# Optimization experiments

Hardware: AMD Instinct MI355X
Metric: run time of the kernel (lower is better)

## Reference

```python
import jax, jax.numpy as jnp
import numpy as np
from jax import lax

# pywt db4 filters (8 taps)
_DEC_LO = np.array([-0.010597401784997278, 0.032883011666982945, 0.030841381835986965,
                    -0.18703481171888114, -0.02798376941698385, 0.6308807679295904,
                    0.7148465705525415, 0.23037781330885523])
_DEC_HI = np.array([-0.23037781330885523, 0.7148465705525415, -0.6308807679295904,
                    -0.02798376941698385, 0.18703481171888114, 0.030841381835986965,
                    -0.032883011666982945, -0.010597401784997278])
_REC_LO = _DEC_LO[::-1].copy()
_REC_HI = _DEC_HI[::-1].copy()
_L = 8  # filter length
LEVELS = 4


def _dwt_level(x):
    # x: (M, n) -> (cA, cD) each (M, (n+_L-1)//2), pywt 'symmetric' mode
    xe = jnp.pad(x, ((0, 0), (_L - 1, _L - 1)), mode='symmetric')[:, 1:]
    ker = jnp.stack([_DEC_LO[::-1], _DEC_HI[::-1]]).astype(x.dtype)[:, None, :]  # (2,1,L)
    y = lax.conv_general_dilated(xe[:, None, :], ker, (2,), 'VALID')  # (M,2,m)
    return y[:, 0], y[:, 1]


def _idwt_level(ca, cd, out_len):
    # inverse DWT, cropped to out_len (matches length of next-finer approximation)
    inp = jnp.stack([ca, cd], axis=1)  # (M,2,m)
    ker = jnp.stack([_REC_LO[::-1], _REC_HI[::-1]]).astype(ca.dtype)[None]  # (1,2,L)
    y = lax.conv_general_dilated(inp, ker, (1,), [(_L - 1, _L - 1)], lhs_dilation=(2,))
    return y[:, 0, _L - 2:_L - 2 + out_len]


def setup_inputs() -> dict:
    key = jax.random.key(0)
    k1, k2, k3, k4 = jax.random.split(key, 4)
    B, N, C = 32, 8192, 64
    m = N
    for _ in range(LEVELS):
        m = (m + _L - 1) // 2  # 518
    scale = 1.0 / (C * C)
    return {
        'x': jax.random.normal(k1, (B, N, C), jnp.float32),
        'w1': scale * jax.random.uniform(k2, (C, C, m), jnp.float32),
        'w2': scale * jax.random.uniform(k3, (C, C, m), jnp.float32),
        'dense_kernel': jax.random.normal(k4, (C, C), jnp.float32) / jnp.sqrt(C).astype(jnp.float32),
        'dense_bias': jnp.zeros((C,), jnp.float32),
    }


def reference(x, w1, w2, dense_kernel, dense_bias):
    B, N, C = x.shape
    xc = jnp.transpose(x, (0, 2, 1)).reshape(B * C, N)  # per-(batch,channel) signals
    # analysis: multi-level DWT
    lens, details = [], []
    a = xc
    for _ in range(LEVELS):
        lens.append(a.shape[1])
        a, d = _dwt_level(a)
        details.append(d)
    m = a.shape[1]
    # channel mixing on coarsest approximation and coarsest detail (WNO kernel)
    a = jnp.einsum('bim,iom->bom', a.reshape(B, C, m), w1).reshape(B * C, m)
    details[-1] = jnp.einsum('bim,iom->bom', details[-1].reshape(B, C, m), w2).reshape(B * C, m)
    # synthesis: multi-level IDWT
    for j in range(LEVELS - 1, -1, -1):
        a = _idwt_level(a, details[j], lens[j])
    y = jnp.transpose(a.reshape(B, C, N), (0, 2, 1))
    shortcut = x @ dense_kernel + dense_bias  # Dense 1x1 shortcut
    out = y + shortcut
    return out * jnp.tanh(jax.nn.softplus(out))  # mish
```

## Files before the change

kernel.cpp:

```cpp
#include <hip/hip_runtime.h>
#include <hip/hip_bf16.h>
#include <stdint.h>

typedef __attribute__((ext_vector_type(8))) short short8;
typedef __attribute__((ext_vector_type(4))) float floatx4;

__device__ __constant__ float c_DL[8] = {
    -0.010597401784997278f, 0.032883011666982945f, 0.030841381835986965f,
    -0.18703481171888114f, -0.02798376941698385f, 0.6308807679295904f,
    0.7148465705525415f, 0.23037781330885523f};
__device__ __constant__ float c_DH[8] = {
    -0.23037781330885523f, 0.7148465705525415f, -0.6308807679295904f,
    -0.02798376941698385f, 0.18703481171888114f, 0.030841381835986965f,
    -0.032883011666982945f, -0.010597401784997278f};
__device__ __constant__ float c_RL[8] = {
    0.23037781330885523f, 0.7148465705525415f, 0.6308807679295904f,
    -0.02798376941698385f, -0.18703481171888114f, 0.030841381835986965f,
    0.032883011666982945f, -0.010597401784997278f};
__device__ __constant__ float c_RH[8] = {
    -0.010597401784997278f, -0.032883011666982945f, 0.030841381835986965f,
    0.18703481171888114f, -0.02798376941698385f, -0.6308807679295904f,
    0.7148465705525415f, -0.23037781330885523f};

__device__ __forceinline__ float bflo(uint32_t u) { return __uint_as_float(u << 16); }
__device__ __forceinline__ float bfhi(uint32_t u) { return __uint_as_float(u & 0xffff0000u); }
__device__ __forceinline__ float ldf(const float* p, size_t i) { return p[i]; }
__device__ __forceinline__ float ldf(const __hip_bfloat16* p, size_t i) { return __bfloat162float(p[i]); }
__device__ __forceinline__ void stf(float* p, size_t i, float v) { p[i] = v; }
__device__ __forceinline__ void stf(__hip_bfloat16* p, size_t i, float v) { p[i] = __float2bfloat16(v); }
__device__ __forceinline__ short f2bs(float f) {
  __hip_bfloat16 h = __float2bfloat16(f);
  return *reinterpret_cast<short*>(&h);
}

__device__ __forceinline__ int reflect_idx(int t, int n) {
  if (t < 0) t = -1 - t;
  if (t >= n) t = 2 * n - 1 - t;
  return t;
}

#define S1R 4100
#define S2R 2056

#define NT1 134
__global__ __launch_bounds__(256) void k_dwt_first(const float* __restrict__ x,
                                                   __hip_bfloat16* __restrict__ outa,
                                                   __hip_bfloat16* __restrict__ outd) {
  const int b = blockIdx.y;
  const int k0 = blockIdx.x * 64;
  const int tid = threadIdx.x;
  __shared__ float xs[NT1 * 65];

  const float4* x4 = (const float4*)x;
  for (int idx = tid; idx < NT1 * 16; idx += 256) {
    int nl = idx >> 4, cq = idx & 15;
    int t = 2 * k0 - 6 + nl;
    int n = reflect_idx(t, 8192);
    float4 v = x4[((size_t)b * 8192 + n) * 16 + cq];
    float* d = &xs[nl * 65 + 4 * cq];
    d[0] = v.x; d[1] = v.y; d[2] = v.z; d[3] = v.w;
  }
  __syncthreads();

  const int kk = tid & 63;
  const int k = k0 + kk;
  if (k >= 4099) return;
  for (int c = (tid >> 6); c < 64; c += 4) {
    float lo = 0.f, hi = 0.f;
#pragma unroll
    for (int j = 0; j < 8; ++j) {
      float v = xs[(2 * kk + 7 - j) * 65 + c];
      lo += c_DL[j] * v;
      hi += c_DH[j] * v;
    }
    size_t s = (size_t)b * 64 + c;
    outa[s * S1R + k] = __float2bfloat16(lo);
    outd[s * S1R + k] = __float2bfloat16(hi);
  }
}

__global__ __launch_bounds__(256) void k_ana234(const __hip_bfloat16* __restrict__ a1,
                                                __hip_bfloat16* __restrict__ d2o,
                                                float* __restrict__ d3o,
                                                float* __restrict__ a4o,
                                                float* __restrict__ d4o) {
  const int r = blockIdx.x;
  const int tid = threadIdx.x;
  __shared__ float s1[4100];
  __shared__ float s2[2054];
  __shared__ float s3[1032];

  const uint2* row2 = (const uint2*)(a1 + (size_t)r * S1R);
  for (int i = tid; i < 1025; i += 256) {
    uint2 u = row2[i];
    int e = 4 * i;
    s1[e] = bflo(u.x); s1[e + 1] = bfhi(u.x);
    s1[e + 2] = bflo(u.y); s1[e + 3] = bfhi(u.y);
  }
  __syncthreads();

  for (int k = tid; k < 2053; k += 256) {
    float lo = 0.f, hi = 0.f;
    if (k >= 3 && k <= 2048) {
      const float2* p = (const float2*)&s1[2 * k - 6];
      float2 v0 = p[0], v1 = p[1], v2 = p[2], v3 = p[3];
      lo = c_RL[0]*v0.x + c_RL[1]*v0.y + c_RL[2]*v1.x + c_RL[3]*v1.y +
           c_RL[4]*v2.x + c_RL[5]*v2.y + c_RL[6]*v3.x + c_RL[7]*v3.y;
      hi = c_RH[0]*v0.x + c_RH[1]*v0.y + c_RH[2]*v1.x + c_RH[3]*v1.y +
           c_RH[4]*v2.x + c_RH[5]*v2.y + c_RH[6]*v3.x + c_RH[7]*v3.y;
    } else {
#pragma unroll
      for (int j = 0; j < 8; ++j) {
        float v = s1[reflect_idx(2 * k + 1 - j, 4099)];
        lo += c_DL[j] * v; hi += c_DH[j] * v;
      }
    }
    d2o[(size_t)r * S2R + k] = __float2bfloat16(hi);
    s2[k] = lo;
  }
  __syncthreads();

  for (int k = tid; k < 1030; k += 256) {
    float lo = 0.f, hi = 0.f;
    if (k >= 3 && k <= 1025) {
      const float2* p = (const float2*)&s2[2 * k - 6];
      float2 v0 = p[0], v1 = p[1], v2 = p[2], v3 = p[3];
      lo = c_RL[0]*v0.x + c_RL[1]*v0.y + c_RL[2]*v1.x + c_RL[3]*v1.y +
           c_RL[4]*v2.x + c_RL[5]*v2.y + c_RL[6]*v3.x + c_RL[7]*v3.y;
      hi = c_RH[0]*v0.x + c_RH[1]*v0.y + c_RH[2]*v1.x + c_RH[3]*v1.y +
           c_RH[4]*v2.x + c_RH[5]*v2.y + c_RH[6]*v3.x + c_RH[7]*v3.y;
    } else {
#pragma unroll
      for (int j = 0; j < 8; ++j) {
        float v = s2[reflect_idx(2 * k + 1 - j, 2053)];
        lo += c_DL[j] * v; hi += c_DH[j] * v;
      }
    }
    d3o[(size_t)r * 1030 + k] = hi;
    s3[k] = lo;
  }
  __syncthreads();

  for (int k = tid; k < 518; k += 256) {
    float lo = 0.f, hi = 0.f;
    if (k >= 3 && k <= 514) {
      const float2* p = (const float2*)&s3[2 * k - 6];
      float2 v0 = p[0], v1 = p[1], v2 = p[2], v3 = p[3];
      lo = c_RL[0]*v0.x + c_RL[1]*v0.y + c_RL[2]*v1.x + c_RL[3]*v1.y +
           c_RL[4]*v2.x + c_RL[5]*v2.y + c_RL[6]*v3.x + c_RL[7]*v3.y;
      hi = c_RH[0]*v0.x + c_RH[1]*v0.y + c_RH[2]*v1.x + c_RH[3]*v1.y +
           c_RH[4]*v2.x + c_RH[5]*v2.y + c_RH[6]*v3.x + c_RH[7]*v3.y;
    } else {
#pragma unroll
      for (int j = 0; j < 8; ++j) {
        float v = s3[reflect_idx(2 * k + 1 - j, 1030)];
        lo += c_DL[j] * v; hi += c_DH[j] * v;
      }
    }
    a4o[(size_t)r * 518 + k] = lo;
    d4o[(size_t)r * 518 + k] = hi;
  }
}

__global__ __launch_bounds__(256) void k_mix_p(const float* __restrict__ a4,
                                               const float* __restrict__ d4,
                                               const float* __restrict__ w1,
                                               const float* __restrict__ w2,
                                               float* __restrict__ am,
                                               float* __restrict__ dm) {
  const int bx = blockIdx.x;
  const int xcd = bx & 7;
  const int j = bx >> 3;
  const int p = (xcd < 6) ? (xcd * 65 + j) : (390 + (xcd - 6) * 64 + j);

  __shared__ float w1s[4096];
  __shared__ float w2s[4096];
  __shared__ float as[2048];
  __shared__ float ds[2048];

  const int tid = threadIdx.x;
  for (int idx = tid; idx < 4096; idx += 256) {
    w1s[idx] = w1[(size_t)idx * 518 + p];
    w2s[idx] = w2[(size_t)idx * 518 + p];
  }
  for (int idx = tid; idx < 2048; idx += 256) {
    int i = idx >> 5, b = idx & 31;
    as[idx] = a4[(size_t)(b * 64 + i) * 518 + p];
    ds[idx] = d4[(size_t)(b * 64 + i) * 518 + p];
  }
  __syncthreads();

  const int o0 = (tid & 15) * 4;
  const int bq = tid >> 4;
  floatx4 acc0 = {0.f, 0.f, 0.f, 0.f}, acc1 = {0.f, 0.f, 0.f, 0.f};
  floatx4 accd0 = {0.f, 0.f, 0.f, 0.f}, accd1 = {0.f, 0.f, 0.f, 0.f};

#pragma unroll 4
  for (int i = 0; i < 64; ++i) {
    floatx4 wv1 = *(const floatx4*)&w1s[i * 64 + o0];
    floatx4 wv2 = *(const floatx4*)&w2s[i * 64 + o0];
    float a0 = as[i * 32 + bq];
    float a1 = as[i * 32 + bq + 16];
    float dv0 = ds[i * 32 + bq];
    float dv1 = ds[i * 32 + bq + 16];
#pragma unroll
    for (int q = 0; q < 4; ++q) {
      acc0[q] += a0 * wv1[q];
      acc1[q] += a1 * wv1[q];
      accd0[q] += dv0 * wv2[q];
      accd1[q] += dv1 * wv2[q];
    }
  }

#pragma unroll
  for (int q = 0; q < 4; ++q) {
    size_t s0 = (size_t)(bq * 64 + o0 + q) * 518 + p;
    size_t s1 = (size_t)((bq + 16) * 64 + o0 + q) * 518 + p;
    am[s0] = acc0[q];
    am[s1] = acc1[q];
    dm[s0] = accd0[q];
    dm[s1] = accd1[q];
  }
}

__global__ __launch_bounds__(256) void k_syn32(const float* __restrict__ a4m,
                                               const float* __restrict__ d4m,
                                               const float* __restrict__ d3,
                                               __hip_bfloat16* __restrict__ r2out) {
  const int r = blockIdx.x;
  const int tid = threadIdx.x;
  __shared__ float sa[518], sd[518], s3d[1030], r3[1030];
  for (int i = tid; i < 518; i += 256) {
    sa[i] = a4m[(size_t)r * 518 + i];
    sd[i] = d4m[(size_t)r * 518 + i];
  }
  for (int i = tid; i < 1030; i += 256) s3d[i] = d3[(size_t)r * 1030 + i];
  __syncthreads();
  for (int s = tid; s < 1030; s += 256) {
    int u = s >> 1, par = s & 1;
    float acc = 0.f;
#pragma unroll
    for (int t = 0; t < 4; ++t) {
      int i = u + 3 - t;
      float fl = par ? c_RL[2 * t + 1] : c_RL[2 * t];
      float fh = par ? c_RH[2 * t + 1] : c_RH[2 * t];
      acc += fl * sa[i] + fh * sd[i];
    }
    r3[s] = acc;
  }
  __syncthreads();
  for (int s = tid; s < 2053; s += 256) {
    int u = s >> 1, par = s & 1;
    float acc = 0.f;
#pragma unroll
    for (int t = 0; t < 4; ++t) {
      int i = u + 3 - t;
      float fl = par ? c_RL[2 * t + 1] : c_RL[2 * t];
      float fh = par ? c_RH[2 * t + 1] : c_RH[2 * t];
      acc += fl * r3[i] + fh * s3d[i];
    }
    r2out[(size_t)r * S2R + s] = __float2bfloat16(acc);
  }
}

template <typename TCa, typename TCd, typename TOut>
__global__ void k_idwt(const TCa* __restrict__ ca, const TCd* __restrict__ cd,
                       TOut* __restrict__ out, int m, int out_len, int sin, int sout) {
  int s = blockIdx.x * blockDim.x + threadIdx.x;
  if (s >= out_len) return;
  const TCa* pa = ca + (size_t)blockIdx.y * sin;
  const TCd* pd = cd + (size_t)blockIdx.y * sin;
  int u = s >> 1, par = s & 1;
  float acc = 0.f;
#pragma unroll
  for (int t = 0; t < 4; ++t) {
    int i = u + 3 - t;
    float fl = par ? c_RL[2 * t + 1] : c_RL[2 * t];
    float fh = par ? c_RH[2 * t + 1] : c_RH[2 * t];
    acc += fl * ldf(pa, i) + fh * ldf(pd, i);
  }
  stf(out, (size_t)blockIdx.y * sout + s, acc);
}

__global__ __launch_bounds__(256) void k_epilogue(const __hip_bfloat16* __restrict__ r1,
                                                  const __hip_bfloat16* __restrict__ dd1,
                                                  const float* __restrict__ x,
                                                  const float* __restrict__ dk,
                                                  const float* __restrict__ bias,
                                                  float* __restrict__ out) {
  const int b = blockIdx.y;
  const int n0 = blockIdx.x * 64;
  const int u0 = n0 >> 1;
  const int tid = threadIdx.x;
  const int lane = tid & 63;
  const int w = tid >> 6;

  __shared__ __hip_bfloat16 Kt[64 * 72];
  __shared__ float ra[35 * 65];
  __shared__ float rd[35 * 65];

  {
    const float4* dk4 = (const float4*)dk;
    for (int idx = tid; idx < 1024; idx += 256) {
      int c = idx >> 4, o0 = (idx & 15) * 4;
      float4 v = dk4[idx];
      Kt[(o0 + 0) * 72 + c] = __float2bfloat16(v.x);
      Kt[(o0 + 1) * 72 + c] = __float2bfloat16(v.y);
      Kt[(o0 + 2) * 72 + c] = __float2bfloat16(v.z);
      Kt[(o0 + 3) * 72 + c] = __float2bfloat16(v.w);
    }
  }
  {
    int o2 = tid >> 2;
    const __hip_bfloat16* pr = r1 + (size_t)(b * 64 + o2) * S1R + u0;
    const __hip_bfloat16* pd = dd1 + (size_t)(b * 64 + o2) * S1R + u0;
    for (int il = (tid & 3); il < 35; il += 4) {
      ra[il * 65 + o2] = __bfloat162float(pr[il]);
      rd[il * 65 + o2] = __bfloat162float(pd[il]);
    }
  }
  __syncthreads();

  const int m16 = lane & 15;
  const int kq = (lane >> 4) * 8;
  const int nrow = w * 16 + m16;
  const float* xrow = x + ((size_t)b * 8192 + n0 + nrow) * 64;

  floatx4 acc[4];
#pragma unroll
  for (int ot = 0; ot < 4; ++ot) acc[ot] = (floatx4){0.f, 0.f, 0.f, 0.f};

#pragma unroll
  for (int ks = 0; ks < 2; ++ks) {
    float4 xa = *(const float4*)(xrow + ks * 32 + kq);
    float4 xb = *(const float4*)(xrow + ks * 32 + kq + 4);
    short8 af;
    af[0] = f2bs(xa.x); af[1] = f2bs(xa.y); af[2] = f2bs(xa.z); af[3] = f2bs(xa.w);
    af[4] = f2bs(xb.x); af[5] = f2bs(xb.y); af[6] = f2bs(xb.z); af[7] = f2bs(xb.w);
#pragma unroll
    for (int ot = 0; ot < 4; ++ot) {
      short8 bf = *(const short8*)&Kt[(ot * 16 + m16) * 72 + ks * 32 + kq];
      acc[ot] = __builtin_amdgcn_mfma_f32_16x16x32_bf16(af, bf, acc[ot], 0, 0, 0);
    }
  }

  const int rbase = (lane >> 4) * 4;
#pragma unroll
  for (int ot = 0; ot < 4; ++ot) {
    int o_loc = ot * 16 + m16;
    float bo = bias[o_loc];
#pragma unroll
    for (int rg = 0; rg < 4; ++rg) {
      int n_loc = w * 16 + rbase + rg;
      int ul = n_loc >> 1, par = n_loc & 1;
      float wv = 0.f;
#pragma unroll
      for (int t = 0; t < 4; ++t) {
        int i = ul + 3 - t;
        float fl = par ? c_RL[2 * t + 1] : c_RL[2 * t];
        float fh = par ? c_RH[2 * t + 1] : c_RH[2 * t];
        wv += fl * ra[i * 65 + o_loc] + fh * rd[i * 65 + o_loc];
      }
      float v = acc[ot][rg] + wv + bo;
      float e = __expf(fminf(v, 15.f));
      float num = e * (e + 2.f);
      float mm = (v > 15.f) ? v : v * (num / (num + 2.f));
      out[((size_t)b * 8192 + n0 + n_loc) * 64 + o_loc] = mm;
    }
  }
}

extern "C" void kernel_launch(void* const* d_in, const int* in_sizes, int n_in,
                              void* d_out, int out_size, void* d_ws, size_t ws_size,
                              hipStream_t stream) {
  const float* x    = (const float*)d_in[0];
  const float* w1   = (const float*)d_in[1];
  const float* w2   = (const float*)d_in[2];
  const float* dk   = (const float*)d_in[3];
  const float* bias = (const float*)d_in[4];
  float* out = (float*)d_out;

  const size_t R = 2048;

  float* wf = (float*)d_ws;
  float* d3f = wf; wf += R * 1030;
  float* a4f = wf; wf += R * 518;
  float* d4f = wf; wf += R * 518;
  float* a4m = wf; wf += R * 518;
  float* d4m = wf; wf += R * 518;
  __hip_bfloat16* wb = (__hip_bfloat16*)wf;
  __hip_bfloat16* a1b = wb; wb += R * S1R;
  __hip_bfloat16* d1b = wb; wb += R * S1R;
  __hip_bfloat16* a2b = wb; wb += R * S2R;
  __hip_bfloat16* d2b = wb; wb += R * S2R;

  k_dwt_first<<<dim3(65, 32), 256, 0, stream>>>(x, a1b, d1b);
  k_ana234<<<dim3(2048), 256, 0, stream>>>(a1b, d2b, d3f, a4f, d4f);
  k_mix_p<<<dim3(518), 256, 0, stream>>>(a4f, d4f, w1, w2, a4m, d4m);
  k_syn32<<<dim3(2048), 256, 0, stream>>>(a4m, d4m, d3f, a2b);
  k_idwt<__hip_bfloat16, __hip_bfloat16, __hip_bfloat16>
      <<<dim3((4099 + 255) / 256, 2048), 256, 0, stream>>>(a2b, d2b, a1b, 2053, 4099, S2R, S1R);
  k_epilogue<<<dim3(128, 32), 256, 0, stream>>>(a1b, d1b, x, dk, bias, out);
}
```

Baseline: 303.6 us.

## Transpose mixing weights and coarse coefficients to mode-major layout for coalesced loads

Adds a kernel that transposes w1/w2 into mode-major (p, i*64+o) layout on every call. The analysis kernel now writes a4/d4 in mode-major order, with a block-index swizzle so writes are grouped. The mixing kernel then loads contiguous float4 rows per mode and is split in two, one half for approximation and one for detail. This replaces stride-518 gathers in the mixing kernel with coalesced reads, at the cost of an extra pass of about 17 MB over the weights each call and strided writes in the analysis kernel.

```diff
diff --git a/kernel.cpp b/kernel.cpp
--- a/kernel.cpp
+++ b/kernel.cpp
@@ -42,6 +42,28 @@
 #define S1R 4100
 #define S2R 2056
 
+__global__ __launch_bounds__(256) void k_wT(const float* __restrict__ w1,
+                                            const float* __restrict__ w2,
+                                            float* __restrict__ wt1,
+                                            float* __restrict__ wt2) {
+  const float* w = blockIdx.z ? w2 : w1;
+  float* wt = blockIdx.z ? wt2 : wt1;
+  const int io0 = blockIdx.x * 64;
+  const int p0 = blockIdx.y * 64;
+  const int pw = min(64, 518 - p0);
+  const int tid = threadIdx.x;
+  __shared__ float ts[64 * 65];
+  for (int idx = tid; idx < 64 * 64; idx += 256) {
+    int row = idx >> 6, col = idx & 63;
+    if (col < pw) ts[row * 65 + col] = w[(size_t)(io0 + row) * 518 + p0 + col];
+  }
+  __syncthreads();
+  for (int idx = tid; idx < 64 * 64; idx += 256) {
+    int pl = idx >> 6, io = idx & 63;
+    if (pl < pw) wt[(size_t)(p0 + pl) * 4096 + io0 + io] = ts[io * 65 + pl];
+  }
+}
+
 #define NT1 134
 __global__ __launch_bounds__(256) void k_dwt_first(const float* __restrict__ x,
                                                    __hip_bfloat16* __restrict__ outa,
@@ -84,7 +106,11 @@
                                                 float* __restrict__ d3o,
                                                 float* __restrict__ a4o,
                                                 float* __restrict__ d4o) {
-  const int r = blockIdx.x;
+  const int bid = blockIdx.x;
+  const int s = (bid & 7) * 256 + (bid >> 3);
+  const int i_ch = s >> 5;
+  const int bb = s & 31;
+  const int r = bb * 64 + i_ch;
   const int tid = threadIdx.x;
   __shared__ float s1[4100];
   __shared__ float s2[2054];
@@ -157,69 +183,58 @@
         lo += c_DL[j] * v; hi += c_DH[j] * v;
       }
     }
-    a4o[(size_t)r * 518 + k] = lo;
-    d4o[(size_t)r * 518 + k] = hi;
-  }
-}
-
-__global__ __launch_bounds__(256) void k_mix_p(const float* __restrict__ a4,
-                                               const float* __restrict__ d4,
-                                               const float* __restrict__ w1,
-                                               const float* __restrict__ w2,
-                                               float* __restrict__ am,
-                                               float* __restrict__ dm) {
+    a4o[(size_t)k * 2048 + s] = lo;
+    d4o[(size_t)k * 2048 + s] = hi;
+  }
+}
+
+__global__ __launch_bounds__(256) void k_mix_pc(const float* __restrict__ wt1,
+                                                const float* __restrict__ wt2,
+                                                const float* __restrict__ a4t,
+                                                const float* __restrict__ d4t,
+                                                float* __restrict__ am,
+                                                float* __restrict__ dm) {
   const int bx = blockIdx.x;
   const int xcd = bx & 7;
   const int j = bx >> 3;
   const int p = (xcd < 6) ? (xcd * 65 + j) : (390 + (xcd - 6) * 64 + j);
 
-  __shared__ float w1s[4096];
-  __shared__ float w2s[4096];
-  __shared__ float as[2048];
-  __shared__ float ds[2048];
-
-  const int tid = threadIdx.x;
-  for (int idx = tid; idx < 4096; idx += 256) {
-    w1s[idx] = w1[(size_t)idx * 518 + p];
-    w2s[idx] = w2[(size_t)idx * 518 + p];
-  }
-  for (int idx = tid; idx < 2048; idx += 256) {
-    int i = idx >> 5, b = idx & 31;
-    as[idx] = a4[(size_t)(b * 64 + i) * 518 + p];
-    ds[idx] = d4[(size_t)(b * 64 + i) * 518 + p];
-  }
+  const float* w = blockIdx.y ? wt2 : wt1;
+  const float* act = blockIdx.y ? d4t : a4t;
+  float* outp = blockIdx.y ? dm : am;
+
+  __shared__ float ws[4096];
+  __shared__ float as_[2048];
+  const int tid = threadIdx.x;
+
+  const float4* wg = (const float4*)(w + (size_t)p * 4096);
+  const float4* ag = (const float4*)(act + (size_t)p * 2048);
+  float4* ws4 = (float4*)ws;
+  float4* as4 = (float4*)as_;
+  for (int t = tid; t < 1024; t += 256) ws4[t] = wg[t];
+  for (int t = tid; t < 512; t += 256) as4[t] = ag[t];
   __syncthreads();
 
   const int o0 = (tid & 15) * 4;
   const int bq = tid >> 4;
   floatx4 acc0 = {0.f, 0.f, 0.f, 0.f}, acc1 = {0.f, 0.f, 0.f, 0.f};
-  floatx4 accd0 = {0.f, 0.f, 0.f, 0.f}, accd1 = {0.f, 0.f, 0.f, 0.f};
-
-#pragma unroll 4
+
+#pragma unroll 8
   for (int i = 0; i < 64; ++i) {
-    floatx4 wv1 = *(const floatx4*)&w1s[i * 64 + o0];
-    floatx4 wv2 = *(const floatx4*)&w2s[i * 64 + o0];
-    float a0 = as[i * 32 + bq];
-    float a1 = as[i * 32 + bq + 16];
-    float dv0 = ds[i * 32 + bq];
-    float dv1 = ds[i * 32 + bq + 16];
+    floatx4 wv = *(const floatx4*)&ws[i * 64 + o0];
+    float a0 = as_[i * 32 + bq];
+    float a1 = as_[i * 32 + bq + 16];
 #pragma unroll
     for (int q = 0; q < 4; ++q) {
-      acc0[q] += a0 * wv1[q];
-      acc1[q] += a1 * wv1[q];
-      accd0[q] += dv0 * wv2[q];
-      accd1[q] += dv1 * wv2[q];
+      acc0[q] += a0 * wv[q];
+      acc1[q] += a1 * wv[q];
     }
   }
 
 #pragma unroll
   for (int q = 0; q < 4; ++q) {
-    size_t s0 = (size_t)(bq * 64 + o0 + q) * 518 + p;
-    size_t s1 = (size_t)((bq + 16) * 64 + o0 + q) * 518 + p;
-    am[s0] = acc0[q];
-    am[s1] = acc1[q];
-    dm[s0] = accd0[q];
-    dm[s1] = accd1[q];
+    outp[(size_t)(bq * 64 + o0 + q) * 518 + p] = acc0[q];
+    outp[(size_t)((bq + 16) * 64 + o0 + q) * 518 + p] = acc1[q];
   }
 }
 
@@ -384,19 +399,22 @@
 
   float* wf = (float*)d_ws;
   float* d3f = wf; wf += R * 1030;
-  float* a4f = wf; wf += R * 518;
-  float* d4f = wf; wf += R * 518;
+  float* a4t = wf; wf += R * 518;
+  float* d4t = wf; wf += R * 518;
   float* a4m = wf; wf += R * 518;
   float* d4m = wf; wf += R * 518;
+  float* wt1 = wf; wf += (size_t)518 * 4096;
+  float* wt2 = wf; wf += (size_t)518 * 4096;
   __hip_bfloat16* wb = (__hip_bfloat16*)wf;
   __hip_bfloat16* a1b = wb; wb += R * S1R;
   __hip_bfloat16* d1b = wb; wb += R * S1R;
   __hip_bfloat16* a2b = wb; wb += R * S2R;
   __hip_bfloat16* d2b = wb; wb += R * S2R;
 
+  k_wT<<<dim3(64, 9, 2), 256, 0, stream>>>(w1, w2, wt1, wt2);
   k_dwt_first<<<dim3(65, 32), 256, 0, stream>>>(x, a1b, d1b);
-  k_ana234<<<dim3(2048), 256, 0, stream>>>(a1b, d2b, d3f, a4f, d4f);
-  k_mix_p<<<dim3(518), 256, 0, stream>>>(a4f, d4f, w1, w2, a4m, d4m);
+  k_ana234<<<dim3(2048), 256, 0, stream>>>(a1b, d2b, d3f, a4t, d4t);
+  k_mix_pc<<<dim3(518, 2), 256, 0, stream>>>(wt1, wt2, a4t, d4t, a4m, d4m);
   k_syn32<<<dim3(2048), 256, 0, stream>>>(a4m, d4m, d3f, a2b);
   k_idwt<__hip_bfloat16, __hip_bfloat16, __hip_bfloat16>
       <<<dim3((4099 + 255) / 256, 2048), 256, 0, stream>>>(a2b, d2b, a1b, 2053, 4099, S2R, S1R);
```

After: 285.1 us. -6.1%, faster.
